# Performance work log

Measured on AMD Instinct MI355X. Metric: run time of the kernel, lower is better.

## Reference

```python
import jax, jax.numpy as jnp
import numpy as np

HIDDEN = 2048
NUM_HEADS = 8
NUM_KV_HEADS = 1
HEAD_DIM = 256
ROPE_THETA = 10000.0
T = 2048  # num tokens (single causal prefill sequence)
Q_SIZE = NUM_HEADS * HEAD_DIM        # 2048
KV_SIZE = NUM_KV_HEADS * HEAD_DIM    # 256


def _apply_rope(x, positions):
    # x: [T, n_heads, head_dim], neox style (rotate halves)
    half = HEAD_DIM // 2
    inv_freq = 1.0 / (ROPE_THETA ** (jnp.arange(half, dtype=jnp.float32) * 2.0 / HEAD_DIM))
    ang = positions.astype(jnp.float32)[:, None] * inv_freq[None, :]   # [T, half]
    cos = jnp.cos(ang)[:, None, :]
    sin = jnp.sin(ang)[:, None, :]
    x1, x2 = jnp.split(x, 2, axis=-1)
    return jnp.concatenate([x1 * cos - x2 * sin, x2 * cos + x1 * sin], axis=-1)


def setup_inputs() -> dict:
    key = jax.random.key(0)
    k1, k2, k3 = jax.random.split(key, 3)
    hidden_states = jax.random.normal(k1, (T, HIDDEN), dtype=jnp.float32)
    Wqkv = jax.random.normal(k2, (Q_SIZE + 2 * KV_SIZE, HIDDEN), dtype=jnp.float32) * 0.02
    Wo = jax.random.normal(k3, (HIDDEN, Q_SIZE), dtype=jnp.float32) * 0.02
    positions = jnp.arange(T, dtype=jnp.int32)
    return {"positions": positions, "hidden_states": hidden_states, "Wqkv": Wqkv, "Wo": Wo}


def reference(positions, hidden_states, Wqkv, Wo):
    scaling = HEAD_DIM ** -0.5
    qkv = hidden_states @ Wqkv.T                                   # [T, Q+2KV]
    q = qkv[:, :Q_SIZE].reshape(T, NUM_HEADS, HEAD_DIM)
    k = qkv[:, Q_SIZE:Q_SIZE + KV_SIZE].reshape(T, NUM_KV_HEADS, HEAD_DIM)
    v = qkv[:, Q_SIZE + KV_SIZE:].reshape(T, NUM_KV_HEADS, HEAD_DIM)
    q = _apply_rope(q, positions)
    k = _apply_rope(k, positions)
    # GQA: group query heads over kv heads
    g = NUM_HEADS // NUM_KV_HEADS
    qg = q.reshape(T, NUM_KV_HEADS, g, HEAD_DIM)
    scores = jnp.einsum('qhgd,khd->hgqk', qg, k) * scaling         # [kv, g, T, T]
    causal = jnp.arange(T)[:, None] >= jnp.arange(T)[None, :]
    scores = jnp.where(causal[None, None], scores, jnp.finfo(scores.dtype).min)
    probs = jax.nn.softmax(scores, axis=-1)
    attn = jnp.einsum('hgqk,khd->qhgd', probs, v).reshape(T, Q_SIZE)
    return attn @ Wo.T
```

## Files before the change

kernel.cpp:

```cpp
#include <hip/hip_runtime.h>
#include <hip/hip_bf16.h>

typedef __bf16 bf16x8 __attribute__((ext_vector_type(8)));
typedef __bf16 bf16x4 __attribute__((ext_vector_type(4)));
typedef float floatx4 __attribute__((ext_vector_type(4)));

__device__ __forceinline__ float fast_exp2(float x) {
    return __builtin_amdgcn_exp2f(x);
}

__device__ __forceinline__ void lds_barrier() {
    asm volatile("s_waitcnt lgkmcnt(0)\n\ts_barrier" ::: "memory");
}

__global__ __launch_bounds__(256) void cast_all(const float* __restrict__ hid,
                                                const float* __restrict__ wqkv,
                                                const float* __restrict__ wo,
                                                __bf16* __restrict__ Ah,
                                                __bf16* __restrict__ Wqkvh,
                                                __bf16* __restrict__ Woh) {
    const int n1 = 1048576, n2 = 1310720;
    int i = blockIdx.x * 256 + threadIdx.x;
    const float* in;
    __bf16* out;
    int j;
    if (i < n1) { in = hid; out = Ah; j = i; }
    else if (i < n1 + n2) { in = wqkv; out = Wqkvh; j = i - n1; }
    else { in = wo; out = Woh; j = i - n1 - n2; }
    float4 v = ((const float4*)in)[j];
    bf16x4 o;
    o[0] = (__bf16)v.x; o[1] = (__bf16)v.y; o[2] = (__bf16)v.z; o[3] = (__bf16)v.w;
    ((bf16x4*)out)[j] = o;
}

__global__ __launch_bounds__(256) void gemm_bt_splitk(const __bf16* __restrict__ A,
                                                      const __bf16* __restrict__ B,
                                                      __bf16* __restrict__ C,
                                                      int M, int N, int K) {
    __shared__ __attribute__((aligned(16))) __bf16 As[128 * 64];
    __shared__ __attribute__((aligned(16))) __bf16 Bs[128 * 64];

    int tid = threadIdx.x, lane = tid & 63, w = tid >> 6;
    int wm = (w >> 1) * 64, wn = (w & 1) * 64;
    int bm0 = blockIdx.x * 128, bn0 = blockIdx.y * 128;
    int r = lane & 15, q4 = lane >> 4;
    int rr = lane >> 2, qq = lane & 3;
    int Khalf = K >> 1;
    int kbase = (int)blockIdx.z * Khalf;

    const __bf16* Agp[4];
    const __bf16* Bgp[4];
    __bf16* Asd[4];
    __bf16* Bsd[4];
#pragma unroll
    for (int j = 0; j < 4; j++) {
        int c = w * 4 + j;
        int kk = c >> 3, g = c & 7;
        Agp[j] = A + (size_t)(bm0 + g * 16 + rr) * K + kbase + kk * 32 + qq * 8;
        Bgp[j] = B + (size_t)(bn0 + g * 16 + rr) * K + kbase + kk * 32 + qq * 8;
        Asd[j] = &As[c * 512 + lane * 8];
        Bsd[j] = &Bs[c * 512 + lane * 8];
    }

    floatx4 acc[4][4];
#pragma unroll
    for (int i = 0; i < 4; i++)
#pragma unroll
        for (int j = 0; j < 4; j++) acc[i][j] = (floatx4)0.f;

    bf16x8 ar[4], br[4];
#pragma unroll
    for (int j = 0; j < 4; j++) {
        ar[j] = *(const bf16x8*)Agp[j];
        br[j] = *(const bf16x8*)Bgp[j];
    }

    for (int k0 = 0; k0 < Khalf; k0 += 64) {
        lds_barrier();
#pragma unroll
        for (int j = 0; j < 4; j++) {
            *(bf16x8*)Asd[j] = ar[j];
            *(bf16x8*)Bsd[j] = br[j];
        }
        if (k0 + 64 < Khalf) {
#pragma unroll
            for (int j = 0; j < 4; j++) {
                ar[j] = *(const bf16x8*)(Agp[j] + k0 + 64);
                br[j] = *(const bf16x8*)(Bgp[j] + k0 + 64);
            }
        }
        lds_barrier();

#pragma unroll
        for (int kk = 0; kk < 2; kk++) {
            bf16x8 a[4], b[4];
#pragma unroll
            for (int mt = 0; mt < 4; mt++)
                a[mt] = *(const bf16x8*)&As[(kk * 8 + (wm >> 4) + mt) * 512 + r * 32 + q4 * 8];
#pragma unroll
            for (int nt = 0; nt < 4; nt++)
                b[nt] = *(const bf16x8*)&Bs[(kk * 8 + (wn >> 4) + nt) * 512 + r * 32 + q4 * 8];
#pragma unroll
            for (int mt = 0; mt < 4; mt++)
#pragma unroll
                for (int nt = 0; nt < 4; nt++)
                    acc[mt][nt] = __builtin_amdgcn_mfma_f32_16x16x32_bf16(a[mt], b[nt], acc[mt][nt], 0, 0, 0);
        }
    }

    __bf16* Cp = C + (size_t)blockIdx.z * M * N;
#pragma unroll
    for (int mt = 0; mt < 4; mt++)
#pragma unroll
        for (int nt = 0; nt < 4; nt++) {
            int row = bm0 + wm + mt * 16 + q4 * 4;
            int col = bn0 + wn + nt * 16 + r;
#pragma unroll
            for (int i = 0; i < 4; i++)
                Cp[(size_t)(row + i) * N + col] = (__bf16)acc[mt][nt][i];
        }
}

__global__ __launch_bounds__(256) void rope_vtrans(const __bf16* __restrict__ qa,
                                                   const __bf16* __restrict__ qb,
                                                   const int* __restrict__ positions,
                                                   __bf16* __restrict__ Qo,
                                                   __bf16* __restrict__ Ko,
                                                   __bf16* __restrict__ Vt) {
    __shared__ float tile[32][33];
    int b = blockIdx.x;
    if (b < 9216) {
        int idx = b * 256 + threadIdx.x;
        int i = idx & 127;
        int th = idx >> 7;
        int head = th % 9;
        int t = th / 9;
        float invf = expf(-(float)i * 0.07195578415606394f);
        float ang = (float)positions[t] * invf;
        float s = sinf(ang), c = cosf(ang);
        size_t off = (size_t)t * 2560 + (head < 8 ? head * 256 : 2048);
        float x1 = (float)qa[off + i] + (float)qb[off + i];
        float x2 = (float)qa[off + i + 128] + (float)qb[off + i + 128];
        if (head < 8) {
            const float qs = 0.09016844f;
            __bf16* dst = Qo + (size_t)t * 2048 + head * 256;
            dst[i]       = (__bf16)((x1 * c - x2 * s) * qs);
            dst[i + 128] = (__bf16)((x2 * c + x1 * s) * qs);
        } else {
            __bf16* dst = Ko + (size_t)t * 256;
            dst[i]       = (__bf16)(x1 * c - x2 * s);
            dst[i + 128] = (__bf16)(x2 * c + x1 * s);
        }
    } else {
        int bb = b - 9216;
        int bt = bb & 63;
        int bc = bb >> 6;
        int tx = threadIdx.x & 31;
        int ty0 = threadIdx.x >> 5;
#pragma unroll
        for (int ty = ty0; ty < 32; ty += 8) {
            size_t gi = (size_t)(bt * 32 + ty) * 2560 + 2304 + bc * 32 + tx;
            tile[ty][tx] = (float)qa[gi] + (float)qb[gi];
        }
        __syncthreads();
#pragma unroll
        for (int ty = ty0; ty < 32; ty += 8)
            Vt[(size_t)bt * 8192 + (bc * 32 + ty) * 32 + tx] = (__bf16)tile[tx][ty];
    }
}

__global__ __launch_bounds__(256) void attn_kernel(const __bf16* __restrict__ Q,
                                                   const __bf16* __restrict__ Kg,
                                                   const __bf16* __restrict__ Vt,
                                                   __bf16* __restrict__ Opart,
                                                   float2* __restrict__ Ml) {
    __shared__ __attribute__((aligned(16))) __bf16 Ks[32 * 264];
    __shared__ __attribute__((aligned(16))) __bf16 Vs[16 * 512];
    __shared__ __attribute__((aligned(16))) __bf16 Ps[4][16][40];

    int hg = blockIdx.x;
    int rs = 407 - (int)blockIdx.y;
    int k, base;
    if (rs < 24)       { k = 1; base = 0; }
    else if (rs < 72)  { k = 2; base = 24; }
    else if (rs < 144) { k = 3; base = 72; }
    else if (rs < 240) { k = 4; base = 144; }
    else if (rs < 360) { k = 5; base = 240; }
    else               { k = 6; base = 360; }
    int idx = rs - base;
    int s = idx % k;
    int g = (k - 1) * 24 + idx / k;
    int slot = base + idx - s;

    int start = s * 384;
    int end = g * 16 + 16;
    if (end > start + 384) end = start + 384;
    int ntiles = (end - start + 31) >> 5;

    int tid = threadIdx.x, lane = tid & 63, w = tid >> 6;
    int r = lane & 15, q4 = lane >> 4;
    int h = hg * 4 + w;

    int krow = w * 8 + (lane & 7);
    int kcol = (lane >> 3) * 32;
    __bf16* kd = &Ks[krow * 264 + kcol];
    __bf16* vd = &Vs[(tid >> 4) * 512 + (tid & 15) * 8];
    const __bf16* vgp = Vt + (size_t)tid * 32;

    bf16x8 qf[8];
    {
        const __bf16* qrow = Q + (size_t)(g * 16 + r) * 2048 + h * 256 + q4 * 8;
#pragma unroll
        for (int ks = 0; ks < 8; ks++) qf[ks] = *(const bf16x8*)(qrow + ks * 32);
    }

    bf16x8 ones;
#pragma unroll
    for (int i = 0; i < 8; i++) ones[i] = (__bf16)1.0f;

    floatx4 acc[16];
#pragma unroll
    for (int i = 0; i < 16; i++) acc[i] = (floatx4)0.f;
    floatx4 acc_l = (floatx4)0.f;

    bf16x8 kr[4], vr[4];
    {
        const __bf16* kp = Kg + (size_t)(start + krow) * 256 + kcol;
        const __bf16* vp = vgp + (size_t)(start >> 5) * 8192;
#pragma unroll
        for (int j = 0; j < 4; j++) {
            kr[j] = *(const bf16x8*)(kp + j * 8);
            vr[j] = *(const bf16x8*)(vp + j * 8);
        }
    }

    for (int t = 0; t < ntiles; t++) {
        int kt0 = start + t * 32;
        lds_barrier();
#pragma unroll
        for (int j = 0; j < 4; j++) {
            *(bf16x8*)(kd + j * 8) = kr[j];
            *(bf16x8*)(vd + j * 128) = vr[j];
        }
        if (t + 1 < ntiles) {
            const __bf16* kp = Kg + (size_t)(kt0 + 32 + krow) * 256 + kcol;
            const __bf16* vp = vgp + (size_t)((kt0 + 32) >> 5) * 8192;
#pragma unroll
            for (int j = 0; j < 4; j++) {
                kr[j] = *(const bf16x8*)(kp + j * 8);
                vr[j] = *(const bf16x8*)(vp + j * 8);
            }
        }
        lds_barrier();

        floatx4 sc[2];
        sc[0] = (floatx4)0.f; sc[1] = (floatx4)0.f;
#pragma unroll
        for (int ks = 0; ks < 8; ks++) {
#pragma unroll
            for (int nt = 0; nt < 2; nt++) {
                bf16x8 kf = *(const bf16x8*)&Ks[(nt * 16 + r) * 264 + ks * 32 + q4 * 8];
                sc[nt] = __builtin_amdgcn_mfma_f32_16x16x32_bf16(qf[ks], kf, sc[nt], 0, 0, 0);
            }
        }
        if (kt0 + 31 > g * 16) {
            int qbase = g * 16 + q4 * 4;
#pragma unroll
            for (int nt = 0; nt < 2; nt++) {
                int kpos = kt0 + nt * 16 + r;
#pragma unroll
                for (int i = 0; i < 4; i++)
                    if (kpos > qbase + i) sc[nt][i] = -3e38f;
            }
        }

#pragma unroll
        for (int nt = 0; nt < 2; nt++)
#pragma unroll
            for (int i = 0; i < 4; i++)
                Ps[w][q4 * 4 + i][(nt * 16 + r) ^ (q4 << 3)] = (__bf16)fast_exp2(sc[nt][i]);
        __builtin_amdgcn_wave_barrier();
        bf16x8 pf = *(const bf16x8*)&Ps[w][r][(q4 * 8) ^ ((r >> 2) << 3)];
        __builtin_amdgcn_wave_barrier();

#pragma unroll
        for (int n16 = 0; n16 < 16; n16++) {
            bf16x8 vf = *(const bf16x8*)&Vs[n16 * 512 + lane * 8];
            acc[n16] = __builtin_amdgcn_mfma_f32_16x16x32_bf16(pf, vf, acc[n16], 0, 0, 0);
        }
        acc_l = __builtin_amdgcn_mfma_f32_16x16x32_bf16(pf, ones, acc_l, 0, 0, 0);
    }

    size_t base_row = (size_t)(slot + s) * 128 + hg * 64 + w * 16;
#pragma unroll
    for (int n16 = 0; n16 < 16; n16++)
#pragma unroll
        for (int i = 0; i < 4; i++)
            Opart[(base_row + q4 * 4 + i) * 256 + n16 * 16 + r] = (__bf16)acc[n16][i];
    if (r == 0) {
#pragma unroll
        for (int i = 0; i < 4; i++)
            Ml[base_row + q4 * 4 + i] = make_float2(0.f, acc_l[i]);
    }
}

__global__ __launch_bounds__(256) void combine_kernel(const __bf16* __restrict__ Opart,
                                                      const float2* __restrict__ Ml,
                                                      __bf16* __restrict__ attnb) {
    int wid = blockIdx.x * 4 + (threadIdx.x >> 6);
    int lane = threadIdx.x & 63;
    int t = wid >> 3, h = wid & 7;
    int g = t >> 4, row = t & 15;
    int hg = h >> 2, w = h & 3;
    int nsp = g / 24 + 1;
    int full = g / 24, rem = g % 24;
    int fg = 12 * full * (full + 1) + rem * (full + 1);

    float ls[6];
    size_t rbase[6];
    for (int s = 0; s < nsp; s++) {
        rbase[s] = (size_t)(fg + s) * 128 + hg * 64 + w * 16 + row;
        ls[s] = Ml[rbase[s]].y;
    }
    float L = 0.f;
    float o[4] = {0.f, 0.f, 0.f, 0.f};
    for (int s = 0; s < nsp; s++) {
        L += ls[s];
        bf16x4 v = *(const bf16x4*)&Opart[rbase[s] * 256 + lane * 4];
#pragma unroll
        for (int j = 0; j < 4; j++) o[j] += (float)v[j];
    }
    float inv = 1.f / L;
    bf16x4 ov;
#pragma unroll
    for (int j = 0; j < 4; j++) ov[j] = (__bf16)(o[j] * inv);
    *(bf16x4*)&attnb[(size_t)t * 2048 + h * 256 + lane * 4] = ov;
}

__global__ __launch_bounds__(256) void add_out(const __bf16* __restrict__ p0,
                                               const __bf16* __restrict__ p1,
                                               float* __restrict__ out, int n4) {
    int i = blockIdx.x * 256 + threadIdx.x;
    if (i < n4) {
        bf16x4 a = ((const bf16x4*)p0)[i];
        bf16x4 b = ((const bf16x4*)p1)[i];
        float4 o;
        o.x = (float)a[0] + (float)b[0];
        o.y = (float)a[1] + (float)b[1];
        o.z = (float)a[2] + (float)b[2];
        o.w = (float)a[3] + (float)b[3];
        ((float4*)out)[i] = o;
    }
}

extern "C" void kernel_launch(void* const* d_in, const int* in_sizes, int n_in,
                              void* d_out, int out_size, void* d_ws, size_t ws_size,
                              hipStream_t stream) {
    const int* positions = (const int*)d_in[0];
    const float* hidden  = (const float*)d_in[1];
    const float* Wqkv    = (const float*)d_in[2];
    const float* Wo      = (const float*)d_in[3];
    float* out = (float*)d_out;

    char* ws = (char*)d_ws;
    const size_t MB = 1024 * 1024;
    __bf16* Ah    = (__bf16*)(ws + 0 * MB);
    __bf16* Woh   = (__bf16*)(ws + 8 * MB);
    __bf16* Qb    = (__bf16*)(ws + 16 * MB);
    __bf16* Kb    = (__bf16*)(ws + 24 * MB);
    __bf16* Vtb   = (__bf16*)(ws + 25 * MB);
    __bf16* Wqkvh = (__bf16*)(ws + 26 * MB);
    __bf16* qkvp  = (__bf16*)(ws + 36 * MB);
    __bf16* qkv_a = qkvp;
    __bf16* qkv_b = qkvp + (size_t)2048 * 2560;
    __bf16* Opart = (__bf16*)(ws + 26 * MB);
    float2* Ml    = (float2*)(ws + 52 * MB);
    __bf16* attnb = Ah;
    __bf16* gp    = (__bf16*)(ws + 26 * MB);

    cast_all<<<13312, 256, 0, stream>>>(hidden, Wqkv, Wo, Ah, Wqkvh, Woh);

    gemm_bt_splitk<<<dim3(16, 20, 2), 256, 0, stream>>>(Ah, Wqkvh, qkvp, 2048, 2560, 2048);

    rope_vtrans<<<9728, 256, 0, stream>>>(qkv_a, qkv_b, positions, Qb, Kb, Vtb);

    attn_kernel<<<dim3(2, 408), 256, 0, stream>>>(Qb, Kb, Vtb, Opart, Ml);
    combine_kernel<<<4096, 256, 0, stream>>>(Opart, Ml, attnb);

    gemm_bt_splitk<<<dim3(16, 16, 2), 256, 0, stream>>>(attnb, Woh, gp, 2048, 2048, 2048);
    add_out<<<4096, 256, 0, stream>>>(gp, gp + (size_t)2048 * 2048, out, 1048576);
}
```

Before: 225.7 us.

## Double query rows per wave and stream K/V tiles directly into LDS

Each attention wave now handles 32 query rows instead of 16, so every K and V fragment read from LDS feeds two MFMAs and the grid is halved. K and V tiles are double-buffered in LDS and filled with global_load_lds direct copies. The K rows are stored XOR-swizzled and V is laid out in the fragment order the kernel reads, which removes the register staging and the padded LDS rows. The combine kernel's split indexing is updated to the new 32-row groups; the cost is higher register pressure, lower block count and more LDS per block.

```diff
diff --git a/kernel.cpp b/kernel.cpp
--- a/kernel.cpp
+++ b/kernel.cpp
@@ -11,6 +11,11 @@
 
 __device__ __forceinline__ void lds_barrier() {
     asm volatile("s_waitcnt lgkmcnt(0)\n\ts_barrier" ::: "memory");
+}
+
+__device__ __forceinline__ void gload16(const __bf16* g, __bf16* l) {
+    __builtin_amdgcn_global_load_lds((const __attribute__((address_space(1))) void*)g,
+                                     (__attribute__((address_space(3))) void*)l, 16, 0, 0);
 }
 
 __global__ __launch_bounds__(256) void cast_all(const float* __restrict__ hid,
@@ -147,9 +152,10 @@
             dst[i]       = (__bf16)((x1 * c - x2 * s) * qs);
             dst[i + 128] = (__bf16)((x2 * c + x1 * s) * qs);
         } else {
+            int sw = (t & 7) << 3;
             __bf16* dst = Ko + (size_t)t * 256;
-            dst[i]       = (__bf16)(x1 * c - x2 * s);
-            dst[i + 128] = (__bf16)(x2 * c + x1 * s);
+            dst[i ^ sw]         = (__bf16)(x1 * c - x2 * s);
+            dst[(i + 128) ^ sw] = (__bf16)(x2 * c + x1 * s);
         }
     } else {
         int bb = b - 9216;
@@ -165,142 +171,161 @@
         __syncthreads();
 #pragma unroll
         for (int ty = ty0; ty < 32; ty += 8)
-            Vt[(size_t)bt * 8192 + (bc * 32 + ty) * 32 + tx] = (__bf16)tile[tx][ty];
-    }
-}
-
-__global__ __launch_bounds__(256) void attn_kernel(const __bf16* __restrict__ Q,
-                                                   const __bf16* __restrict__ Kg,
-                                                   const __bf16* __restrict__ Vt,
-                                                   __bf16* __restrict__ Opart,
-                                                   float2* __restrict__ Ml) {
-    __shared__ __attribute__((aligned(16))) __bf16 Ks[32 * 264];
-    __shared__ __attribute__((aligned(16))) __bf16 Vs[16 * 512];
-    __shared__ __attribute__((aligned(16))) __bf16 Ps[4][16][40];
+            Vt[(size_t)bt * 8192 + (bc * 2 + (ty >> 4)) * 512 + (ty & 15) * 8
+               + (tx >> 3) * 128 + (tx & 7)] = (__bf16)tile[tx][ty];
+    }
+}
+
+__global__ __launch_bounds__(256, 2) void attn_kernel(const __bf16* __restrict__ Q,
+                                                      const __bf16* __restrict__ Kg,
+                                                      const __bf16* __restrict__ Vt,
+                                                      __bf16* __restrict__ Opart,
+                                                      float2* __restrict__ Ml) {
+    __shared__ __attribute__((aligned(16))) __bf16 Ks[2][32 * 256];
+    __shared__ __attribute__((aligned(16))) __bf16 Vs[2][16 * 512];
+    __shared__ __attribute__((aligned(16))) __bf16 Ps[4][32][40];
 
     int hg = blockIdx.x;
-    int rs = 407 - (int)blockIdx.y;
+    int rs = 203 - (int)blockIdx.y;
     int k, base;
-    if (rs < 24)       { k = 1; base = 0; }
-    else if (rs < 72)  { k = 2; base = 24; }
-    else if (rs < 144) { k = 3; base = 72; }
-    else if (rs < 240) { k = 4; base = 144; }
-    else if (rs < 360) { k = 5; base = 240; }
-    else               { k = 6; base = 360; }
+    if (rs < 12)       { k = 1; base = 0; }
+    else if (rs < 36)  { k = 2; base = 12; }
+    else if (rs < 72)  { k = 3; base = 36; }
+    else if (rs < 120) { k = 4; base = 72; }
+    else if (rs < 180) { k = 5; base = 120; }
+    else               { k = 6; base = 180; }
     int idx = rs - base;
     int s = idx % k;
-    int g = (k - 1) * 24 + idx / k;
+    int g = (k - 1) * 12 + idx / k;
     int slot = base + idx - s;
 
     int start = s * 384;
-    int end = g * 16 + 16;
+    int end = g * 32 + 32;
     if (end > start + 384) end = start + 384;
-    int ntiles = (end - start + 31) >> 5;
+    int ntiles = (end - start) >> 5;
 
     int tid = threadIdx.x, lane = tid & 63, w = tid >> 6;
     int r = lane & 15, q4 = lane >> 4;
     int h = hg * 4 + w;
-
-    int krow = w * 8 + (lane & 7);
-    int kcol = (lane >> 3) * 32;
-    __bf16* kd = &Ks[krow * 264 + kcol];
-    __bf16* vd = &Vs[(tid >> 4) * 512 + (tid & 15) * 8];
-    const __bf16* vgp = Vt + (size_t)tid * 32;
-
-    bf16x8 qf[8];
+    int sw = (r & 7) << 3;
+
+    bf16x8 qf[2][8];
+#pragma unroll
+    for (int qt = 0; qt < 2; qt++) {
+        const __bf16* qrow = Q + (size_t)(g * 32 + qt * 16 + r) * 2048 + h * 256 + q4 * 8;
+#pragma unroll
+        for (int ks = 0; ks < 8; ks++) qf[qt][ks] = *(const bf16x8*)(qrow + ks * 32);
+    }
+
+    bf16x8 ones;
+#pragma unroll
+    for (int i = 0; i < 8; i++) ones[i] = (__bf16)1.0f;
+
+    floatx4 acc[2][16];
+#pragma unroll
+    for (int qt = 0; qt < 2; qt++)
+#pragma unroll
+        for (int i = 0; i < 16; i++) acc[qt][i] = (floatx4)0.f;
+    floatx4 acc_l[2];
+    acc_l[0] = (floatx4)0.f; acc_l[1] = (floatx4)0.f;
+
     {
-        const __bf16* qrow = Q + (size_t)(g * 16 + r) * 2048 + h * 256 + q4 * 8;
-#pragma unroll
-        for (int ks = 0; ks < 8; ks++) qf[ks] = *(const bf16x8*)(qrow + ks * 32);
-    }
-
-    bf16x8 ones;
-#pragma unroll
-    for (int i = 0; i < 8; i++) ones[i] = (__bf16)1.0f;
-
-    floatx4 acc[16];
-#pragma unroll
-    for (int i = 0; i < 16; i++) acc[i] = (floatx4)0.f;
-    floatx4 acc_l = (floatx4)0.f;
-
-    bf16x8 kr[4], vr[4];
-    {
-        const __bf16* kp = Kg + (size_t)(start + krow) * 256 + kcol;
-        const __bf16* vp = vgp + (size_t)(start >> 5) * 8192;
+        const __bf16* kp = Kg + (size_t)start * 256 + tid * 8;
+        const __bf16* vp = Vt + (size_t)(start >> 5) * 8192 + tid * 8;
+        __bf16* kl = &Ks[0][tid * 8];
+        __bf16* vl = &Vs[0][tid * 8];
 #pragma unroll
         for (int j = 0; j < 4; j++) {
-            kr[j] = *(const bf16x8*)(kp + j * 8);
-            vr[j] = *(const bf16x8*)(vp + j * 8);
+            gload16(kp + j * 2048, kl + j * 2048);
+            gload16(vp + j * 2048, vl + j * 2048);
         }
     }
 
     for (int t = 0; t < ntiles; t++) {
+        int cb = t & 1;
         int kt0 = start + t * 32;
-        lds_barrier();
-#pragma unroll
-        for (int j = 0; j < 4; j++) {
-            *(bf16x8*)(kd + j * 8) = kr[j];
-            *(bf16x8*)(vd + j * 128) = vr[j];
-        }
+        asm volatile("s_barrier" ::: "memory");
         if (t + 1 < ntiles) {
-            const __bf16* kp = Kg + (size_t)(kt0 + 32 + krow) * 256 + kcol;
-            const __bf16* vp = vgp + (size_t)((kt0 + 32) >> 5) * 8192;
+            int kt1 = kt0 + 32;
+            const __bf16* kp = Kg + (size_t)kt1 * 256 + tid * 8;
+            const __bf16* vp = Vt + (size_t)(kt1 >> 5) * 8192 + tid * 8;
+            __bf16* kl = &Ks[cb ^ 1][tid * 8];
+            __bf16* vl = &Vs[cb ^ 1][tid * 8];
 #pragma unroll
             for (int j = 0; j < 4; j++) {
-                kr[j] = *(const bf16x8*)(kp + j * 8);
-                vr[j] = *(const bf16x8*)(vp + j * 8);
+                gload16(kp + j * 2048, kl + j * 2048);
+                gload16(vp + j * 2048, vl + j * 2048);
             }
-        }
-        lds_barrier();
-
-        floatx4 sc[2];
-        sc[0] = (floatx4)0.f; sc[1] = (floatx4)0.f;
+            asm volatile("s_waitcnt vmcnt(8)\n\ts_barrier" ::: "memory");
+        } else {
+            asm volatile("s_waitcnt vmcnt(0)\n\ts_barrier" ::: "memory");
+        }
+
+        floatx4 sc[2][2];
+        sc[0][0] = (floatx4)0.f; sc[0][1] = (floatx4)0.f;
+        sc[1][0] = (floatx4)0.f; sc[1][1] = (floatx4)0.f;
 #pragma unroll
         for (int ks = 0; ks < 8; ks++) {
 #pragma unroll
             for (int nt = 0; nt < 2; nt++) {
-                bf16x8 kf = *(const bf16x8*)&Ks[(nt * 16 + r) * 264 + ks * 32 + q4 * 8];
-                sc[nt] = __builtin_amdgcn_mfma_f32_16x16x32_bf16(qf[ks], kf, sc[nt], 0, 0, 0);
+                bf16x8 kf = *(const bf16x8*)&Ks[cb][(nt * 16 + r) * 256 + ((ks * 32 + q4 * 8) ^ sw)];
+#pragma unroll
+                for (int qt = 0; qt < 2; qt++)
+                    sc[qt][nt] = __builtin_amdgcn_mfma_f32_16x16x32_bf16(qf[qt][ks], kf, sc[qt][nt], 0, 0, 0);
             }
         }
-        if (kt0 + 31 > g * 16) {
-            int qbase = g * 16 + q4 * 4;
-#pragma unroll
-            for (int nt = 0; nt < 2; nt++) {
-                int kpos = kt0 + nt * 16 + r;
+        if (kt0 + 31 > g * 32) {
+#pragma unroll
+            for (int qt = 0; qt < 2; qt++) {
+                int qbase = g * 32 + qt * 16 + q4 * 4;
+#pragma unroll
+                for (int nt = 0; nt < 2; nt++) {
+                    int kpos = kt0 + nt * 16 + r;
+#pragma unroll
+                    for (int i = 0; i < 4; i++)
+                        if (kpos > qbase + i) sc[qt][nt][i] = -3e38f;
+                }
+            }
+        }
+
+#pragma unroll
+        for (int qt = 0; qt < 2; qt++)
+#pragma unroll
+            for (int nt = 0; nt < 2; nt++)
 #pragma unroll
                 for (int i = 0; i < 4; i++)
-                    if (kpos > qbase + i) sc[nt][i] = -3e38f;
-            }
-        }
-
-#pragma unroll
-        for (int nt = 0; nt < 2; nt++)
+                    Ps[w][qt * 16 + q4 * 4 + i][(nt * 16 + r) ^ (q4 << 3)] = (__bf16)fast_exp2(sc[qt][nt][i]);
+        __builtin_amdgcn_wave_barrier();
+        bf16x8 pf[2];
+#pragma unroll
+        for (int qt = 0; qt < 2; qt++)
+            pf[qt] = *(const bf16x8*)&Ps[w][qt * 16 + r][(q4 * 8) ^ ((r >> 2) << 3)];
+        __builtin_amdgcn_wave_barrier();
+
+#pragma unroll
+        for (int n16 = 0; n16 < 16; n16++) {
+            bf16x8 vf = *(const bf16x8*)&Vs[cb][n16 * 512 + lane * 8];
+            acc[0][n16] = __builtin_amdgcn_mfma_f32_16x16x32_bf16(pf[0], vf, acc[0][n16], 0, 0, 0);
+            acc[1][n16] = __builtin_amdgcn_mfma_f32_16x16x32_bf16(pf[1], vf, acc[1][n16], 0, 0, 0);
+        }
+        acc_l[0] = __builtin_amdgcn_mfma_f32_16x16x32_bf16(pf[0], ones, acc_l[0], 0, 0, 0);
+        acc_l[1] = __builtin_amdgcn_mfma_f32_16x16x32_bf16(pf[1], ones, acc_l[1], 0, 0, 0);
+    }
+
+    size_t base_row = (size_t)(slot + s) * 256 + hg * 128 + w * 32;
+#pragma unroll
+    for (int qt = 0; qt < 2; qt++)
+#pragma unroll
+        for (int n16 = 0; n16 < 16; n16++)
 #pragma unroll
             for (int i = 0; i < 4; i++)
-                Ps[w][q4 * 4 + i][(nt * 16 + r) ^ (q4 << 3)] = (__bf16)fast_exp2(sc[nt][i]);
-        __builtin_amdgcn_wave_barrier();
-        bf16x8 pf = *(const bf16x8*)&Ps[w][r][(q4 * 8) ^ ((r >> 2) << 3)];
-        __builtin_amdgcn_wave_barrier();
-
-#pragma unroll
-        for (int n16 = 0; n16 < 16; n16++) {
-            bf16x8 vf = *(const bf16x8*)&Vs[n16 * 512 + lane * 8];
-            acc[n16] = __builtin_amdgcn_mfma_f32_16x16x32_bf16(pf, vf, acc[n16], 0, 0, 0);
-        }
-        acc_l = __builtin_amdgcn_mfma_f32_16x16x32_bf16(pf, ones, acc_l, 0, 0, 0);
-    }
-
-    size_t base_row = (size_t)(slot + s) * 128 + hg * 64 + w * 16;
-#pragma unroll
-    for (int n16 = 0; n16 < 16; n16++)
-#pragma unroll
-        for (int i = 0; i < 4; i++)
-            Opart[(base_row + q4 * 4 + i) * 256 + n16 * 16 + r] = (__bf16)acc[n16][i];
+                Opart[(base_row + qt * 16 + q4 * 4 + i) * 256 + n16 * 16 + r] = (__bf16)acc[qt][n16][i];
     if (r == 0) {
 #pragma unroll
-        for (int i = 0; i < 4; i++)
-            Ml[base_row + q4 * 4 + i] = make_float2(0.f, acc_l[i]);
+        for (int qt = 0; qt < 2; qt++)
+#pragma unroll
+            for (int i = 0; i < 4; i++)
+                Ml[base_row + qt * 16 + q4 * 4 + i] = make_float2(0.f, acc_l[qt][i]);
     }
 }
 
@@ -310,21 +335,21 @@
     int wid = blockIdx.x * 4 + (threadIdx.x >> 6);
     int lane = threadIdx.x & 63;
     int t = wid >> 3, h = wid & 7;
-    int g = t >> 4, row = t & 15;
+    int g = t >> 5, r32 = t & 31;
+    int qt = r32 >> 4, row16 = r32 & 15;
     int hg = h >> 2, w = h & 3;
-    int nsp = g / 24 + 1;
-    int full = g / 24, rem = g % 24;
-    int fg = 12 * full * (full + 1) + rem * (full + 1);
+    int k = g / 12 + 1;
+    int fg = 6 * k * (k - 1) + (g - 12 * (k - 1)) * k;
 
     float ls[6];
     size_t rbase[6];
-    for (int s = 0; s < nsp; s++) {
-        rbase[s] = (size_t)(fg + s) * 128 + hg * 64 + w * 16 + row;
+    for (int s = 0; s < k; s++) {
+        rbase[s] = (size_t)(fg + s) * 256 + hg * 128 + w * 32 + qt * 16 + row16;
         ls[s] = Ml[rbase[s]].y;
     }
     float L = 0.f;
     float o[4] = {0.f, 0.f, 0.f, 0.f};
-    for (int s = 0; s < nsp; s++) {
+    for (int s = 0; s < k; s++) {
         L += ls[s];
         bf16x4 v = *(const bf16x4*)&Opart[rbase[s] * 256 + lane * 4];
 #pragma unroll
@@ -384,7 +409,7 @@
 
     rope_vtrans<<<9728, 256, 0, stream>>>(qkv_a, qkv_b, positions, Qb, Kb, Vtb);
 
-    attn_kernel<<<dim3(2, 408), 256, 0, stream>>>(Qb, Kb, Vtb, Opart, Ml);
+    attn_kernel<<<dim3(2, 204), 256, 0, stream>>>(Qb, Kb, Vtb, Opart, Ml);
     combine_kernel<<<4096, 256, 0, stream>>>(Opart, Ml, attnb);
 
     gemm_bt_splitk<<<dim3(16, 16, 2), 256, 0, stream>>>(attnb, Woh, gp, 2048, 2048, 2048);
```

Measured after the change: 213.2 us. -5.5%, faster.
